# Kernel tuning notes

Hardware: AMD Instinct MI355X
Metric: run time of the kernel (lower is better)

## Reference

```python
import jax, jax.numpy as jnp
import numpy as np

EPS_DIST = 1e-7  # matches torch: log((d+1)/(d+1e-7))


def _cdist(x, p):
    # x: (B, N, D), p: (P, D) -> (B, N, P) Euclidean distances
    x2 = jnp.sum(x * x, axis=-1, keepdims=True)        # (B, N, 1)
    p2 = jnp.sum(p * p, axis=-1)                       # (P,)
    d2 = x2 + p2[None, None, :] - 2.0 * jnp.einsum('bnd,pd->bnp', x, p)
    return jnp.sqrt(jnp.maximum(d2, 1e-12))


def setup_inputs() -> dict:
    key = jax.random.key(0)
    k1, k2, k3 = jax.random.split(key, 3)
    B, C, H, W = 32, 2048, 14, 14
    num_classes, npc = 200, 10
    P = num_classes * npc
    x = jax.random.normal(k1, (B, C, H, W), dtype=jnp.float32)
    prototypes = jax.random.normal(k2, (1, P, C), dtype=jnp.float32)
    fc_w = jax.random.normal(k3, (num_classes, P), dtype=jnp.float32) * 0.02
    return {"x": x, "prototypes": prototypes, "fc_w": fc_w}


def reference(x, prototypes, fc_w):
    B, C, H, W = x.shape
    feats = x.reshape(B, C, H * W).transpose(0, 2, 1)   # (B, HW, D)
    protos = prototypes[0]                              # (P, D)
    num_classes = fc_w.shape[0]
    npc = protos.shape[0] // num_classes

    distances = _cdist(feats, protos)                   # (B, HW, P)
    similarity = jnp.log((distances + 1.0) / (distances + EPS_DIST))
    max_similarity = jnp.max(similarity, axis=1)        # (B, P)
    min_distances = jnp.min(distances, axis=1)          # (B, P)
    min_distances_per_class = min_distances.reshape(B, num_classes, npc)
    scores = max_similarity @ fc_w.T                    # (B, num_classes)
    return scores, min_distances_per_class
```

## Files before the change

### kernel.cpp

```cpp
#include <hip/hip_runtime.h>

#define INF_BITS 0x7F800000u
#define AS1 __attribute__((address_space(1)))
#define AS3 __attribute__((address_space(3)))

typedef float f32x4 __attribute__((ext_vector_type(4)));
typedef __bf16 bf16x8 __attribute__((ext_vector_type(8)));
typedef unsigned short u16x8 __attribute__((ext_vector_type(8)));
typedef unsigned int u32x4 __attribute__((ext_vector_type(4)));

static __device__ __forceinline__ unsigned short f2bf(float f) {
  unsigned int u = __float_as_uint(f);
  return (unsigned short)((u + 0x7FFFu + ((u >> 16) & 1u)) >> 16);
}

__global__ void k_init(unsigned int* __restrict__ outu, u32x4* __restrict__ xTpad,
                       unsigned int* __restrict__ x2u) {
  int i = blockIdx.x * blockDim.x + threadIdx.x;
  if (i < 64000) outu[6400 + i] = INF_BITS;
  if (i < 32768) xTpad[i] = (u32x4){0u, 0u, 0u, 0u};
  if (i < 128) x2u[6272 + i] = INF_BITS;
}

__global__ __launch_bounds__(256) void k_prep_p(const float* __restrict__ protos,
                                                unsigned short* __restrict__ pT,
                                                float* __restrict__ p2) {
  const int row = blockIdx.x;
  const int tid = threadIdx.x;
  __shared__ float red[4];
  float s = 0.f;
  u16x8 h = (u16x8){0, 0, 0, 0, 0, 0, 0, 0};
  if (row < 2000) {
    const float* src = protos + (size_t)row * 2048 + tid * 8;
    f32x4 a = *(const f32x4*)src;
    f32x4 c = *(const f32x4*)(src + 4);
    h = (u16x8){f2bf(a.x), f2bf(a.y), f2bf(a.z), f2bf(a.w),
                f2bf(c.x), f2bf(c.y), f2bf(c.z), f2bf(c.w)};
    s = a.x * a.x + a.y * a.y + a.z * a.z + a.w * a.w +
        c.x * c.x + c.y * c.y + c.z * c.z + c.w * c.w;
  }
  *(u16x8*)(pT + (size_t)row * 2048 + tid * 8) = h;
  #pragma unroll
  for (int off = 32; off; off >>= 1) s += __shfl_xor(s, off);
  if ((tid & 63) == 0) red[tid >> 6] = s;
  __syncthreads();
  if (tid == 0) p2[row] = red[0] + red[1] + red[2] + red[3];
}

__global__ __launch_bounds__(256) void k_prep_x(const float* __restrict__ x,
                                                unsigned short* __restrict__ xT,
                                                float* __restrict__ x2p) {
  const int kt = blockIdx.x;
  const int b  = blockIdx.y;
  const int tid = threadIdx.x;
  __shared__ unsigned short Ls[64][201];
  const float* src = x + ((size_t)b * 2048 + (size_t)kt * 64) * 196;
  for (int idx = tid; idx < 64 * 196; idx += 256) {
    int kk = idx / 196, n = idx - kk * 196;
    Ls[kk][n] = f2bf(src[idx]);
  }
  __syncthreads();
  if (tid < 196) {
    float s = 0.f;
    #pragma unroll
    for (int j = 0; j < 64; ++j) {
      float v = __uint_as_float((unsigned int)Ls[j][tid] << 16);
      s += v * v;
    }
    x2p[kt * 6272 + b * 196 + tid] = s;
  }
  unsigned short* dstb = xT + (size_t)b * 196 * 2048 + kt * 64;
  for (int idx = tid; idx < 196 * 32; idx += 256) {
    int n = idx >> 5, j = idx & 31;
    unsigned int v = (unsigned int)Ls[2 * j][n] |
                     ((unsigned int)Ls[2 * j + 1][n] << 16);
    *(unsigned int*)(dstb + (size_t)n * 2048 + 2 * j) = v;
  }
}

__global__ void k_x2r(const float* __restrict__ x2p, float* __restrict__ x2) {
  int i = blockIdx.x * blockDim.x + threadIdx.x;
  if (i >= 6272) return;
  float s = 0.f;
  #pragma unroll
  for (int c = 0; c < 32; ++c) s += x2p[c * 6272 + i];
  x2[i] = s;
}

__global__ __launch_bounds__(512, 2) void k_main(
    const unsigned short* __restrict__ pT, const unsigned short* __restrict__ xT,
    const float* __restrict__ p2, const float* __restrict__ x2,
    unsigned int* __restrict__ outu) {
  const int orig = blockIdx.x;
  const int wgid = (orig & 7) * 25 + (orig >> 3);
  const int ptpair = wgid / 50;
  const int rem = wgid - ptpair * 50;
  const int ptile = ptpair * 2 + (rem & 1);
  const int mtile = rem >> 1;
  const int p0 = ptile * 256;
  const int m0 = mtile * 256;
  const int tid = threadIdx.x;
  const int lane = tid & 63;
  const int w = tid >> 6;
  const int wp = w >> 2;
  const int wn = w & 3;
  const int lr = lane & 15;
  const int lg = lane >> 4;

  __shared__ __align__(16) char S[131072];

  f32x4 acc[8][4];
  #pragma unroll
  for (int mi = 0; mi < 8; ++mi)
    #pragma unroll
    for (int ni = 0; ni < 4; ++ni)
      acc[mi][ni] = (f32x4){0.f, 0.f, 0.f, 0.f};

  const int rowbase = tid >> 3;
  const int chunk = (tid & 7) ^ (rowbase & 7);
  const char* gA = (const char*)pT + (size_t)(p0 + rowbase) * 4096 + chunk * 16;
  const char* gB = (const char*)xT + (size_t)(m0 + rowbase) * 4096 + chunk * 16;
  const int wbase = w * 1024;

#define STAGE_A(c_, kt_, h_) do {                                              \
    const char* s_ = gA + (size_t)((h_) * 128 * 4096) + (size_t)(kt_) * 128;   \
    _Pragma("unroll")                                                          \
    for (int j_ = 0; j_ < 2; ++j_)                                             \
      __builtin_amdgcn_global_load_lds(                                        \
          (const AS1 void*)(s_ + (size_t)j_ * 64 * 4096),                      \
          (AS3 void*)(S + (c_) * 32768 + (h_) * 16384 + j_ * 8192 + wbase),    \
          16, 0, 0);                                                           \
  } while (0)
#define STAGE_B(c_, kt_, h_) do {                                              \
    const char* s_ = gB + (size_t)((h_) * 128 * 4096) + (size_t)(kt_) * 128;   \
    _Pragma("unroll")                                                          \
    for (int j_ = 0; j_ < 2; ++j_)                                             \
      __builtin_amdgcn_global_load_lds(                                        \
          (const AS1 void*)(s_ + (size_t)j_ * 64 * 4096),                      \
          (AS3 void*)(S + 65536 + (c_) * 32768 + (h_) * 16384 + j_ * 8192 + wbase), \
          16, 0, 0);                                                           \
  } while (0)

  const int swz = ((lr & 7) << 4);
  const int arow = (wp * 128 + lr) * 128;
  const int brow = (wn * 64 + lr) * 128;
  const int koff0 = (lg * 16) ^ swz;
  const int koff1 = (64 + lg * 16) ^ swz;

#define READ_A(dst_, c_, ko_, hf_)                                             \
    _Pragma("unroll")                                                          \
    for (int mi_ = 0; mi_ < 4; ++mi_)                                          \
      dst_[mi_] = *(const bf16x8*)(S + (c_) * 32768 + arow + (hf_) * 8192 +    \
                                   mi_ * 2048 + (ko_));
#define READ_B(dst_, c_, ko_)                                                  \
    _Pragma("unroll")                                                          \
    for (int ni_ = 0; ni_ < 4; ++ni_)                                          \
      dst_[ni_] = *(const bf16x8*)(S + 65536 + (c_) * 32768 + brow +           \
                                   ni_ * 2048 + (ko_));

#define PH_BAR() do { __builtin_amdgcn_sched_barrier(0);                       \
    __builtin_amdgcn_s_barrier(); __builtin_amdgcn_sched_barrier(0); } while (0)
#define LGKM0() do { asm volatile("s_waitcnt lgkmcnt(0)" ::: "memory");        \
    __builtin_amdgcn_sched_barrier(0); } while (0)
#define MFMA_Q(mlo_, af_, bf_) do { __builtin_amdgcn_s_setprio(1);             \
    _Pragma("unroll")                                                          \
    for (int mi_ = (mlo_); mi_ < (mlo_) + 4; ++mi_)                            \
      _Pragma("unroll")                                                        \
      for (int ni_ = 0; ni_ < 4; ++ni_)                                        \
        acc[mi_][ni_] = __builtin_amdgcn_mfma_f32_16x16x32_bf16(               \
            af_[mi_ - (mlo_)], bf_[ni_], acc[mi_][ni_], 0, 0, 0);              \
    __builtin_amdgcn_s_setprio(0); } while (0)

#define KT_BODY(kt_, c_, sa_, sb_, vm_) do {                                   \
    bf16x8 alo[4], ahi[4], bk0[4], bk1[4];                                     \
                                  \
    READ_A(alo, c_, koff0, 0);                                                 \
    READ_B(bk0, c_, koff0);                                                    \
    if (sa_) STAGE_A((c_) ^ 1, (kt_) + 1, 0);                                  \
    PH_BAR(); LGKM0();                                                         \
    MFMA_Q(0, alo, bk0);                                                       \
    PH_BAR();                                                                  \
                                  \
    READ_A(ahi, c_, koff0, 1);                                                 \
    READ_B(bk1, c_, koff1);                                                    \
    if (sa_) STAGE_A((c_) ^ 1, (kt_) + 1, 1);                                  \
    PH_BAR(); LGKM0();                                                         \
    MFMA_Q(4, ahi, bk0);                                                       \
    PH_BAR();                                                                  \
          \
    READ_A(alo, c_, koff1, 0);                                                 \
    if (sb_) STAGE_B(c_, (kt_) + 2, 0);                                        \
    PH_BAR(); LGKM0();                                                         \
    MFMA_Q(0, alo, bk1);                                                       \
    PH_BAR();                                                                  \
                          \
    READ_A(ahi, c_, koff1, 1);                                                 \
    if (sb_) STAGE_B(c_, (kt_) + 2, 1);                                        \
    if ((vm_) == 4)      asm volatile("s_waitcnt vmcnt(4)" ::: "memory");      \
    else if ((vm_) == 0) asm volatile("s_waitcnt vmcnt(0)" ::: "memory");      \
    __builtin_amdgcn_sched_barrier(0);                                         \
    PH_BAR(); LGKM0();                                                         \
    MFMA_Q(4, ahi, bk1);                                                       \
    PH_BAR();                                                                  \
  } while (0)

  STAGE_B(0, 0, 0); STAGE_B(0, 0, 1);
  STAGE_A(0, 0, 0); STAGE_A(0, 0, 1);
  STAGE_B(1, 1, 0); STAGE_B(1, 1, 1);
  asm volatile("s_waitcnt vmcnt(4)" ::: "memory");
  __builtin_amdgcn_sched_barrier(0);
  __builtin_amdgcn_s_barrier();
  __builtin_amdgcn_sched_barrier(0);

  #pragma unroll 1
  for (int it = 0; it < 15; ++it) {
    KT_BODY(2 * it, 0, 1, 1, 4);
    KT_BODY(2 * it + 1, 1, 1, 1, 4);
  }
  KT_BODY(30, 0, 1, 0, 0);
  KT_BODY(31, 1, 0, 0, -1);
#undef KT_BODY
#undef MFMA_Q
#undef READ_A
#undef READ_B
#undef STAGE_A
#undef STAGE_B

  const int wm_base = m0 + wn * 64;
  const int b_lo = wm_base / 196;
  int b_hi = (wm_base + 63) / 196;
  if (b_hi > 31) b_hi = 31;
  const bool wave_ok = (b_lo < 32);
  float x2v[4];
  int seg0[4];
  #pragma unroll
  for (int ni = 0; ni < 4; ++ni) {
    const int m = wm_base + ni * 16 + lr;
    x2v[ni] = x2[m];
    seg0[ni] = ((m / 196) == b_lo);
  }
  const float INF = __uint_as_float(INF_BITS);
  #pragma unroll
  for (int mi = 0; mi < 8; ++mi) {
    const int prow = p0 + wp * 128 + mi * 16 + 4 * lg;
    #pragma unroll
    for (int j = 0; j < 4; ++j) {
      const int p = prow + j;
      const float pp = p2[p];
      float ma = INF, mb = INF;
      #pragma unroll
      for (int ni = 0; ni < 4; ++ni) {
        const float d2 = x2v[ni] + pp - 2.f * acc[mi][ni][j];
        ma = fminf(ma, seg0[ni] ? d2 : INF);
        mb = fminf(mb, seg0[ni] ? INF : d2);
      }
      #pragma unroll
      for (int off = 1; off < 16; off <<= 1) {
        ma = fminf(ma, __shfl_xor(ma, off));
        mb = fminf(mb, __shfl_xor(mb, off));
      }
      if (lr == 0 && p < 2000 && wave_ok) {
        atomicMin(&outu[6400 + b_lo * 2000 + p], __float_as_uint(fmaxf(ma, 0.f)));
        if (b_hi != b_lo)
          atomicMin(&outu[6400 + b_hi * 2000 + p], __float_as_uint(fmaxf(mb, 0.f)));
      }
    }
  }
}

__global__ void k_post(float* __restrict__ out, float* __restrict__ simbuf) {
  int i = blockIdx.x * blockDim.x + threadIdx.x;
  if (i >= 64000) return;
  float d2 = out[6400 + i];
  float d = sqrtf(fmaxf(d2, 1e-12f));
  out[6400 + i] = d;
  simbuf[i] = logf((d + 1.0f) / (d + 1e-7f));
}

__global__ __launch_bounds__(256) void k_scores(const float* __restrict__ fc_w,
                                                const float* __restrict__ simbuf,
                                                float* __restrict__ out) {
  const int id = blockIdx.x * 4 + (threadIdx.x >> 6);
  const int lane = threadIdx.x & 63;
  const int b = id / 200;
  const int c = id - b * 200;
  const f32x4* sv = (const f32x4*)(simbuf + (size_t)b * 2000);
  const f32x4* wv = (const f32x4*)(fc_w + (size_t)c * 2000);
  float s = 0.f;
  #pragma unroll
  for (int it = 0; it < 8; ++it) {
    int i = lane + it * 64;
    if (i < 500) {
      f32x4 a = sv[i], w4 = wv[i];
      s += a.x * w4.x + a.y * w4.y + a.z * w4.z + a.w * w4.w;
    }
  }
  #pragma unroll
  for (int off = 32; off; off >>= 1) s += __shfl_xor(s, off);
  if (lane == 0) out[b * 200 + c] = s;
}

extern "C" void kernel_launch(void* const* d_in, const int* in_sizes, int n_in,
                              void* d_out, int out_size, void* d_ws, size_t ws_size,
                              hipStream_t stream) {
  const float* x      = (const float*)d_in[0];
  const float* protos = (const float*)d_in[1];
  const float* fc_w   = (const float*)d_in[2];
  float* out = (float*)d_out;

  char* wsb = (char*)d_ws;
  unsigned short* pT = (unsigned short*)wsb;
  unsigned short* xT = (unsigned short*)(wsb + 8388608);
  float* p2   = (float*)(wsb + 34603008);
  float* x2   = (float*)(wsb + 34611200);
  float* x2p  = (float*)(wsb + 34636800);
  float* simb = (float*)(wsb + 34636800);

  k_init<<<256, 256, 0, stream>>>((unsigned int*)d_out,
                                  (u32x4*)(wsb + 8388608 + (size_t)6272 * 4096),
                                  (unsigned int*)x2);
  k_prep_p<<<2048, 256, 0, stream>>>(protos, pT, p2);
  k_prep_x<<<dim3(32, 32), 256, 0, stream>>>(x, xT, x2p);
  k_x2r<<<25, 256, 0, stream>>>(x2p, x2);
  k_main<<<200, 512, 0, stream>>>(pT, xT, p2, x2, (unsigned int*)d_out);
  k_post<<<250, 256, 0, stream>>>(out, simb);
  k_scores<<<1600, 256, 0, stream>>>(fc_w, simb, out);
}
```

Measured before the change: 102.4 us.

## Restructure GEMM k-tile body into two phases with full A fragment reads

Each k-tile goes from four read/MFMA phases of 16 MFMAs to two phases of 32 MFMAs, reading all eight A fragments at once. All A staging now issues in the first phase and B staging moves after the final barrier. The wait changes from vmcnt(4) to a full vmcnt(0) each tile. This cuts the barrier count per tile in half but raises register pressure and reduces overlap between global loads and compute.

Result: slower. 109.0 us (+6.5%).

```diff
diff --git a/kernel.cpp b/kernel.cpp
--- a/kernel.cpp
+++ b/kernel.cpp
@@ -147,11 +147,11 @@
   const int koff0 = (lg * 16) ^ swz;
   const int koff1 = (64 + lg * 16) ^ swz;
 
-#define READ_A(dst_, c_, ko_, hf_)                                             \
-    _Pragma("unroll")                                                          \
-    for (int mi_ = 0; mi_ < 4; ++mi_)                                          \
-      dst_[mi_] = *(const bf16x8*)(S + (c_) * 32768 + arow + (hf_) * 8192 +    \
-                                   mi_ * 2048 + (ko_));
+#define READ_A8(dst_, c_, ko_)                                                 \
+    _Pragma("unroll")                                                          \
+    for (int mi_ = 0; mi_ < 8; ++mi_)                                          \
+      dst_[mi_] = *(const bf16x8*)(S + (c_) * 32768 + arow + (mi_ >> 2) * 8192 \
+                                   + (mi_ & 3) * 2048 + (ko_));
 #define READ_B(dst_, c_, ko_)                                                  \
     _Pragma("unroll")                                                          \
     for (int ni_ = 0; ni_ < 4; ++ni_)                                          \
@@ -162,50 +162,35 @@
     __builtin_amdgcn_s_barrier(); __builtin_amdgcn_sched_barrier(0); } while (0)
 #define LGKM0() do { asm volatile("s_waitcnt lgkmcnt(0)" ::: "memory");        \
     __builtin_amdgcn_sched_barrier(0); } while (0)
-#define MFMA_Q(mlo_, af_, bf_) do { __builtin_amdgcn_s_setprio(1);             \
-    _Pragma("unroll")                                                          \
-    for (int mi_ = (mlo_); mi_ < (mlo_) + 4; ++mi_)                            \
+#define MFMA_ALL(af_, bf_) do { __builtin_amdgcn_s_setprio(1);                 \
+    _Pragma("unroll")                                                          \
+    for (int mi_ = 0; mi_ < 8; ++mi_)                                          \
       _Pragma("unroll")                                                        \
       for (int ni_ = 0; ni_ < 4; ++ni_)                                        \
         acc[mi_][ni_] = __builtin_amdgcn_mfma_f32_16x16x32_bf16(               \
-            af_[mi_ - (mlo_)], bf_[ni_], acc[mi_][ni_], 0, 0, 0);              \
+            af_[mi_], bf_[ni_], acc[mi_][ni_], 0, 0, 0);                       \
     __builtin_amdgcn_s_setprio(0); } while (0)
 
 #define KT_BODY(kt_, c_, sa_, sb_, vm_) do {                                   \
-    bf16x8 alo[4], ahi[4], bk0[4], bk1[4];                                     \
-                                  \
-    READ_A(alo, c_, koff0, 0);                                                 \
-    READ_B(bk0, c_, koff0);                                                    \
-    if (sa_) STAGE_A((c_) ^ 1, (kt_) + 1, 0);                                  \
+    bf16x8 a8[8], bb[4];                                                       \
+    READ_A8(a8, c_, koff0);                                                    \
+    READ_B(bb, c_, koff0);                                                     \
+    if (sa_) { STAGE_A((c_) ^ 1, (kt_) + 1, 0); STAGE_A((c_) ^ 1, (kt_) + 1, 1); } \
     PH_BAR(); LGKM0();                                                         \
-    MFMA_Q(0, alo, bk0);                                                       \
+    MFMA_ALL(a8, bb);                                                          \
     PH_BAR();                                                                  \
-                                  \
-    READ_A(ahi, c_, koff0, 1);                                                 \
-    READ_B(bk1, c_, koff1);                                                    \
-    if (sa_) STAGE_A((c_) ^ 1, (kt_) + 1, 1);                                  \
+    READ_A8(a8, c_, koff1);                                                    \
+    READ_B(bb, c_, koff1);                                                     \
     PH_BAR(); LGKM0();                                                         \
-    MFMA_Q(4, ahi, bk0);                                                       \
+    MFMA_ALL(a8, bb);                                                          \
+    if ((vm_) == 0) { asm volatile("s_waitcnt vmcnt(0)" ::: "memory");         \
+      __builtin_amdgcn_sched_barrier(0); }                                     \
     PH_BAR();                                                                  \
-          \
-    READ_A(alo, c_, koff1, 0);                                                 \
-    if (sb_) STAGE_B(c_, (kt_) + 2, 0);                                        \
-    PH_BAR(); LGKM0();                                                         \
-    MFMA_Q(0, alo, bk1);                                                       \
-    PH_BAR();                                                                  \
-                          \
-    READ_A(ahi, c_, koff1, 1);                                                 \
-    if (sb_) STAGE_B(c_, (kt_) + 2, 1);                                        \
-    if ((vm_) == 4)      asm volatile("s_waitcnt vmcnt(4)" ::: "memory");      \
-    else if ((vm_) == 0) asm volatile("s_waitcnt vmcnt(0)" ::: "memory");      \
-    __builtin_amdgcn_sched_barrier(0);                                         \
-    PH_BAR(); LGKM0();                                                         \
-    MFMA_Q(4, ahi, bk1);                                                       \
-    PH_BAR();                                                                  \
+    if (sb_) { STAGE_B(c_, (kt_) + 2, 0); STAGE_B(c_, (kt_) + 2, 1); }         \
   } while (0)
 
+  STAGE_A(0, 0, 0); STAGE_A(0, 0, 1);
   STAGE_B(0, 0, 0); STAGE_B(0, 0, 1);
-  STAGE_A(0, 0, 0); STAGE_A(0, 0, 1);
   STAGE_B(1, 1, 0); STAGE_B(1, 1, 1);
   asm volatile("s_waitcnt vmcnt(4)" ::: "memory");
   __builtin_amdgcn_sched_barrier(0);
@@ -214,14 +199,14 @@
 
   #pragma unroll 1
   for (int it = 0; it < 15; ++it) {
-    KT_BODY(2 * it, 0, 1, 1, 4);
-    KT_BODY(2 * it + 1, 1, 1, 1, 4);
+    KT_BODY(2 * it, 0, 1, 1, 0);
+    KT_BODY(2 * it + 1, 1, 1, 1, 0);
   }
   KT_BODY(30, 0, 1, 0, 0);
   KT_BODY(31, 1, 0, 0, -1);
 #undef KT_BODY
-#undef MFMA_Q
-#undef READ_A
+#undef MFMA_ALL
+#undef READ_A8
 #undef READ_B
 #undef STAGE_A
 #undef STAGE_B
```

## Fold init into prep kernels, vectorize x transpose, fuse post and scores

Applied to the files above, without the earlier changes.

Removes the separate init kernel by moving the output INF fill into k_prep_p and the xT padding and x2 sentinel into an extra row of k_prep_x blocks. Vectorizes the k_prep_x global loads (float4) and the transposed stores (16-byte), and pads the LDS row from 201 to 204 elements. Merges the post (sqrt/log) and scores kernels into one kernel per batch that keeps similarities in shared memory, which cuts two launches in total and the simbuf round trip. The fused scores kernel runs only 32 blocks, so each thread does a serial 250-iteration dot product, which may reduce parallelism.

After: 151.8 us. +48.3%, slower.

```diff
diff --git a/kernel.cpp b/kernel.cpp
--- a/kernel.cpp
+++ b/kernel.cpp
@@ -6,6 +6,7 @@
 
 typedef float f32x4 __attribute__((ext_vector_type(4)));
 typedef __bf16 bf16x8 __attribute__((ext_vector_type(8)));
+typedef unsigned short u16x4 __attribute__((ext_vector_type(4)));
 typedef unsigned short u16x8 __attribute__((ext_vector_type(8)));
 typedef unsigned int u32x4 __attribute__((ext_vector_type(4)));
 
@@ -14,19 +15,14 @@
   return (unsigned short)((u + 0x7FFFu + ((u >> 16) & 1u)) >> 16);
 }
 
-__global__ void k_init(unsigned int* __restrict__ outu, u32x4* __restrict__ xTpad,
-                       unsigned int* __restrict__ x2u) {
-  int i = blockIdx.x * blockDim.x + threadIdx.x;
-  if (i < 64000) outu[6400 + i] = INF_BITS;
-  if (i < 32768) xTpad[i] = (u32x4){0u, 0u, 0u, 0u};
-  if (i < 128) x2u[6272 + i] = INF_BITS;
-}
-
 __global__ __launch_bounds__(256) void k_prep_p(const float* __restrict__ protos,
                                                 unsigned short* __restrict__ pT,
-                                                float* __restrict__ p2) {
+                                                float* __restrict__ p2,
+                                                unsigned int* __restrict__ outu) {
   const int row = blockIdx.x;
   const int tid = threadIdx.x;
+  const int gi = row * 256 + tid;
+  if (gi < 64000) outu[6400 + gi] = INF_BITS;
   __shared__ float red[4];
   float s = 0.f;
   u16x8 h = (u16x8){0, 0, 0, 0, 0, 0, 0, 0};
@@ -49,15 +45,25 @@
 
 __global__ __launch_bounds__(256) void k_prep_x(const float* __restrict__ x,
                                                 unsigned short* __restrict__ xT,
-                                                float* __restrict__ x2p) {
+                                                float* __restrict__ x2p,
+                                                float* __restrict__ x2) {
   const int kt = blockIdx.x;
   const int b  = blockIdx.y;
   const int tid = threadIdx.x;
-  __shared__ unsigned short Ls[64][201];
+  if (b == 32) {
+    u32x4* pad = (u32x4*)(xT + (size_t)6272 * 2048);
+    #pragma unroll
+    for (int j = tid; j < 1024; j += 256)
+      pad[kt * 1024 + j] = (u32x4){0u, 0u, 0u, 0u};
+    if (kt == 0 && tid < 128) x2[6272 + tid] = __uint_as_float(INF_BITS);
+    return;
+  }
+  __shared__ unsigned short Ls[64][204];
   const float* src = x + ((size_t)b * 2048 + (size_t)kt * 64) * 196;
-  for (int idx = tid; idx < 64 * 196; idx += 256) {
-    int kk = idx / 196, n = idx - kk * 196;
-    Ls[kk][n] = f2bf(src[idx]);
+  for (int idx = tid; idx < 3136; idx += 256) {
+    const int kk = idx / 49, c4 = idx - kk * 49;
+    f32x4 v = *(const f32x4*)(src + (size_t)kk * 196 + c4 * 4);
+    *(u16x4*)&Ls[kk][c4 * 4] = (u16x4){f2bf(v.x), f2bf(v.y), f2bf(v.z), f2bf(v.w)};
   }
   __syncthreads();
   if (tid < 196) {
@@ -70,11 +76,15 @@
     x2p[kt * 6272 + b * 196 + tid] = s;
   }
   unsigned short* dstb = xT + (size_t)b * 196 * 2048 + kt * 64;
-  for (int idx = tid; idx < 196 * 32; idx += 256) {
-    int n = idx >> 5, j = idx & 31;
-    unsigned int v = (unsigned int)Ls[2 * j][n] |
-                     ((unsigned int)Ls[2 * j + 1][n] << 16);
-    *(unsigned int*)(dstb + (size_t)n * 2048 + 2 * j) = v;
+  for (int idx = tid; idx < 1568; idx += 256) {
+    const int n = idx >> 3, q = idx & 7;
+    const int k0 = q * 8;
+    u32x4 v;
+    v.x = (unsigned int)Ls[k0 + 0][n] | ((unsigned int)Ls[k0 + 1][n] << 16);
+    v.y = (unsigned int)Ls[k0 + 2][n] | ((unsigned int)Ls[k0 + 3][n] << 16);
+    v.z = (unsigned int)Ls[k0 + 4][n] | ((unsigned int)Ls[k0 + 5][n] << 16);
+    v.w = (unsigned int)Ls[k0 + 6][n] | ((unsigned int)Ls[k0 + 7][n] << 16);
+    *(u32x4*)(dstb + (size_t)n * 2048 + k0) = v;
   }
 }
 
@@ -173,27 +183,23 @@
 
 #define KT_BODY(kt_, c_, sa_, sb_, vm_) do {                                   \
     bf16x8 alo[4], ahi[4], bk0[4], bk1[4];                                     \
-                                  \
     READ_A(alo, c_, koff0, 0);                                                 \
     READ_B(bk0, c_, koff0);                                                    \
     if (sa_) STAGE_A((c_) ^ 1, (kt_) + 1, 0);                                  \
     PH_BAR(); LGKM0();                                                         \
     MFMA_Q(0, alo, bk0);                                                       \
     PH_BAR();                                                                  \
-                                  \
     READ_A(ahi, c_, koff0, 1);                                                 \
     READ_B(bk1, c_, koff1);                                                    \
     if (sa_) STAGE_A((c_) ^ 1, (kt_) + 1, 1);                                  \
     PH_BAR(); LGKM0();                                                         \
     MFMA_Q(4, ahi, bk0);                                                       \
     PH_BAR();                                                                  \
-          \
     READ_A(alo, c_, koff1, 0);                                                 \
     if (sb_) STAGE_B(c_, (kt_) + 2, 0);                                        \
     PH_BAR(); LGKM0();                                                         \
     MFMA_Q(0, alo, bk1);                                                       \
     PH_BAR();                                                                  \
-                          \
     READ_A(ahi, c_, koff1, 1);                                                 \
     if (sb_) STAGE_B(c_, (kt_) + 2, 1);                                        \
     if ((vm_) == 4)      asm volatile("s_waitcnt vmcnt(4)" ::: "memory");      \
@@ -268,36 +274,31 @@
   }
 }
 
-__global__ void k_post(float* __restrict__ out, float* __restrict__ simbuf) {
-  int i = blockIdx.x * blockDim.x + threadIdx.x;
-  if (i >= 64000) return;
-  float d2 = out[6400 + i];
-  float d = sqrtf(fmaxf(d2, 1e-12f));
-  out[6400 + i] = d;
-  simbuf[i] = logf((d + 1.0f) / (d + 1e-7f));
-}
-
-__global__ __launch_bounds__(256) void k_scores(const float* __restrict__ fc_w,
-                                                const float* __restrict__ simbuf,
-                                                float* __restrict__ out) {
-  const int id = blockIdx.x * 4 + (threadIdx.x >> 6);
-  const int lane = threadIdx.x & 63;
-  const int b = id / 200;
-  const int c = id - b * 200;
-  const f32x4* sv = (const f32x4*)(simbuf + (size_t)b * 2000);
-  const f32x4* wv = (const f32x4*)(fc_w + (size_t)c * 2000);
-  float s = 0.f;
-  #pragma unroll
-  for (int it = 0; it < 8; ++it) {
-    int i = lane + it * 64;
-    if (i < 500) {
+__global__ __launch_bounds__(512) void k_postscores(const float* __restrict__ fc_w,
+                                                    float* __restrict__ out) {
+  const int b = blockIdx.x;
+  const int tid = threadIdx.x;
+  __shared__ float sim[2000];
+  for (int p = tid; p < 2000; p += 512) {
+    float d2 = out[6400 + b * 2000 + p];
+    float d = sqrtf(fmaxf(d2, 1e-12f));
+    out[6400 + b * 2000 + p] = d;
+    sim[p] = logf((d + 1.0f) / (d + 1e-7f));
+  }
+  __syncthreads();
+  if (tid < 400) {
+    const int c = tid >> 1, h = tid & 1;
+    const f32x4* sv = (const f32x4*)(sim + h * 1000);
+    const f32x4* wv = (const f32x4*)(fc_w + (size_t)c * 2000 + h * 1000);
+    float s = 0.f;
+    #pragma unroll 4
+    for (int i = 0; i < 250; ++i) {
       f32x4 a = sv[i], w4 = wv[i];
       s += a.x * w4.x + a.y * w4.y + a.z * w4.z + a.w * w4.w;
     }
-  }
-  #pragma unroll
-  for (int off = 32; off; off >>= 1) s += __shfl_xor(s, off);
-  if (lane == 0) out[b * 200 + c] = s;
+    s += __shfl_xor(s, 1);
+    if (h == 0) out[b * 200 + c] = s;
+  }
 }
 
 extern "C" void kernel_launch(void* const* d_in, const int* in_sizes, int n_in,
@@ -314,15 +315,10 @@
   float* p2   = (float*)(wsb + 34603008);
   float* x2   = (float*)(wsb + 34611200);
   float* x2p  = (float*)(wsb + 34636800);
-  float* simb = (float*)(wsb + 34636800);
-
-  k_init<<<256, 256, 0, stream>>>((unsigned int*)d_out,
-                                  (u32x4*)(wsb + 8388608 + (size_t)6272 * 4096),
-                                  (unsigned int*)x2);
-  k_prep_p<<<2048, 256, 0, stream>>>(protos, pT, p2);
-  k_prep_x<<<dim3(32, 32), 256, 0, stream>>>(x, xT, x2p);
+
+  k_prep_p<<<2048, 256, 0, stream>>>(protos, pT, p2, (unsigned int*)d_out);
+  k_prep_x<<<dim3(32, 33), 256, 0, stream>>>(x, xT, x2p, x2);
   k_x2r<<<25, 256, 0, stream>>>(x2p, x2);
   k_main<<<200, 512, 0, stream>>>(pT, xT, p2, x2, (unsigned int*)d_out);
-  k_post<<<250, 256, 0, stream>>>(out, simb);
-  k_scores<<<1600, 256, 0, stream>>>(fc_w, simb, out);
-}
+  k_postscores<<<32, 512, 0, stream>>>(fc_w, out);
+}
```
